# Kernel tuning notes

Hardware: AMD Instinct MI355X
Metric: run time of the kernel (lower is better)

The kernel has to match this reference:

```python
import jax, jax.numpy as jnp
import numpy as np

MODEL_DIM = 256
DK = 32        # dim_per_head
H = 16         # num_heads
HD = DK * H    # 512


def setup_inputs() -> dict:
    key = jax.random.key(0)
    ks = jax.random.split(key, 12)
    B, S = 16, 1024
    sc = 1.0 / np.sqrt(MODEL_DIM)
    inp = {
        "key0":   jax.random.normal(ks[0], (B, S, MODEL_DIM), jnp.float32),
        "value0": jax.random.normal(ks[1], (B, S, MODEL_DIM), jnp.float32),
        "query0": jax.random.normal(ks[2], (B, S, MODEL_DIM), jnp.float32),
        # linear weights stored as [in, out] (torch W.T)
        "Wk": jax.random.normal(ks[3], (MODEL_DIM, HD), jnp.float32) * sc,
        "bk": jax.random.normal(ks[4], (HD,), jnp.float32) * sc,
        "Wv": jax.random.normal(ks[5], (MODEL_DIM, HD), jnp.float32) * sc,
        "bv": jax.random.normal(ks[6], (HD,), jnp.float32) * sc,
        "Wq": jax.random.normal(ks[7], (MODEL_DIM, HD), jnp.float32) * sc,
        "bq": jax.random.normal(ks[8], (HD,), jnp.float32) * sc,
        "Wr": jax.random.normal(ks[9], (MODEL_DIM, HD), jnp.float32) * sc,
        "br": jax.random.normal(ks[10], (HD,), jnp.float32) * sc,
    }
    return inp


def reference(key0, value0, query0, Wk, bk, Wv, bv, Wq, bq, Wr, br):
    B = key0.shape[0]
    k = key0 @ Wk + bk      # [B, S, HD]
    v = value0 @ Wv + bv
    q = query0 @ Wq + bq
    # Faithful to the torch code: plain view (NO transpose) into (B*H, S, DK)
    k = k.reshape(B * H, -1, DK)
    v = v.reshape(B * H, -1, DK)
    q = q.reshape(B * H, -1, DK)
    # scale = (dk // num_heads) ** -0.5 = (32//16)**-0.5 (quirk preserved)
    scale = jnp.asarray((DK // H) ** (-0.5), k.dtype)
    attn = jax.nn.softmax(jnp.einsum("bqd,bkd->bqk", q, k) * scale, axis=2)
    context = jnp.einsum("bqk,bkd->bqd", attn, v)  # [B*H, S, DK]
    context = context.reshape(B, -1, HD)
    residual = (query0 @ Wr + br).reshape(B, -1, HD)
    return jax.nn.relu(residual + context)
```

## Files before the change

kernel.cpp:

```cpp
#include <hip/hip_runtime.h>
#include <hip/hip_bf16.h>

typedef _Float16 f16x8 __attribute__((ext_vector_type(8)));
typedef _Float16 f16x2 __attribute__((ext_vector_type(2)));
typedef float f32x4 __attribute__((ext_vector_type(4)));
typedef float f32x16 __attribute__((ext_vector_type(16)));
typedef unsigned int u32x2 __attribute__((ext_vector_type(2)));
typedef unsigned int u32x4 __attribute__((ext_vector_type(4)));
typedef unsigned short us8 __attribute__((ext_vector_type(8)));

#define GLDS16(gp, lp)                                                        \
  __builtin_amdgcn_global_load_lds(                                           \
      (const __attribute__((address_space(1))) void*)(gp),                    \
      (__attribute__((address_space(3))) void*)(lp), 16, 0, 0)

__device__ __forceinline__ unsigned short f2h(float f) {
  _Float16 h = (_Float16)f;
  return __builtin_bit_cast(unsigned short, h);
}
__device__ __forceinline__ float h2f(unsigned short u) {
  return (float)__builtin_bit_cast(_Float16, u);
}
__device__ __forceinline__ unsigned int pk2(float a, float b) {
  return __builtin_bit_cast(unsigned int, __builtin_amdgcn_cvt_pkrtz(a, b));
}

__global__ __launch_bounds__(256) void k_convert_w(
    const float* __restrict__ Wk, const float* __restrict__ Wv,
    const float* __restrict__ Wq, const float* __restrict__ Wr,
    unsigned short* __restrict__ WT) {
  int o = blockIdx.x * 256 + threadIdx.x;
  int mat = o >> 17, rem = o & 131071;
  int n = rem >> 8, k = rem & 255;
  const float* W = mat == 0 ? Wk : mat == 1 ? Wv : mat == 2 ? Wq : Wr;
  WT[o] = f2h(W[k * 512 + n]);
}

__global__ __launch_bounds__(1024) void k_gemm(
    const float* __restrict__ k0, const float* __restrict__ v0,
    const float* __restrict__ q0, const unsigned short* __restrict__ WT,
    const float* __restrict__ bk, const float* __restrict__ bv,
    const float* __restrict__ bq, const float* __restrict__ br,
    unsigned short* __restrict__ Kb, unsigned short* __restrict__ Vh,
    unsigned short* __restrict__ Qb, unsigned short* __restrict__ Rh) {
  const float CS = 0.70710678118654752f * 1.44269504088896341f;
  int b = blockIdx.x;
  int mat = b >> 7, my = b & 127;
  const float* A = mat == 0 ? k0 : mat == 1 ? v0 : q0;
  const unsigned short* Wm = WT + mat * 131072;
  const float* bias = mat == 0 ? bk : mat == 1 ? bv : mat == 2 ? bq : br;
  unsigned short* C = mat == 0 ? Kb : mat == 1 ? Vh : mat == 2 ? Qb : Rh;
  __shared__ __align__(16) unsigned short As[2][4096];
  __shared__ __align__(16) unsigned short Bs[2][16384];
  int m0 = my * 128;
  int tid = threadIdx.x, lane = tid & 63, w = tid >> 6;
  int wm = w >> 3, wn = w & 7, q = lane & 15, hi = lane >> 4;
  f32x4 acc[4][4];
#pragma unroll
  for (int i = 0; i < 4; ++i)
#pragma unroll
    for (int j = 0; j < 4; ++j) acc[i][j] = f32x4{0.f, 0.f, 0.f, 0.f};

  float bsv[4];
#pragma unroll
  for (int j = 0; j < 4; ++j) bsv[j] = bias[wn * 64 + j * 16 + q];

  const float* gA = A + (m0 + (tid >> 3)) * 256 + (tid & 7) * 4;
  const unsigned short* gB = Wm + (tid >> 2) * 256 + (tid & 3) * 8;

  float4 arF[2];
  arF[0] = *(const float4*)gA;
  arF[1] = *(const float4*)(gA + 32);
  GLDS16(gB, &Bs[0][tid * 8]);
  GLDS16(gB + 65536, &Bs[0][8192 + tid * 8]);
  asm volatile("s_waitcnt vmcnt(3)" ::: "memory");
  *(u32x2*)&As[0][tid * 4] =
      u32x2{pk2(arF[0].x, arF[0].y), pk2(arF[0].z, arF[0].w)};
  asm volatile("s_waitcnt lgkmcnt(0)" ::: "memory");
  __builtin_amdgcn_s_barrier();
  __builtin_amdgcn_sched_barrier(0);

#pragma unroll
  for (int kt = 0; kt < 8; ++kt) {
    int cur = kt & 1, nxt = cur ^ 1;
    if (kt < 6) arF[cur] = *(const float4*)(gA + (kt + 2) * 32);
    if (kt < 7) {
      GLDS16(gB + (kt + 1) * 32, &Bs[nxt][tid * 8]);
      GLDS16(gB + (kt + 1) * 32 + 65536, &Bs[nxt][8192 + tid * 8]);
    }
    if (kt < 6) asm volatile("s_waitcnt vmcnt(3)" ::: "memory");
    else if (kt == 6) asm volatile("s_waitcnt vmcnt(2)" ::: "memory");
    else asm volatile("s_waitcnt vmcnt(0)" ::: "memory");
    __builtin_amdgcn_s_barrier();
    __builtin_amdgcn_sched_barrier(0);

    f16x8 af[4], bf[4];
#pragma unroll
    for (int i = 0; i < 4; ++i)
      af[i] = *(const f16x8*)&As[cur][(wm * 64 + i * 16 + q) * 32 + hi * 8];
#pragma unroll
    for (int j = 0; j < 4; ++j)
      bf[j] = *(const f16x8*)&Bs[cur][(wn * 64 + j * 16 + q) * 32 + hi * 8];
#pragma unroll
    for (int i = 0; i < 4; ++i)
#pragma unroll
      for (int j = 0; j < 4; ++j)
        acc[i][j] = __builtin_amdgcn_mfma_f32_16x16x32_f16(af[i], bf[j], acc[i][j], 0, 0, 0);

    if (kt < 7) {
      *(u32x2*)&As[nxt][tid * 4] =
          u32x2{pk2(arF[nxt].x, arF[nxt].y), pk2(arF[nxt].z, arF[nxt].w)};
    }
    asm volatile("s_waitcnt lgkmcnt(0)" ::: "memory");
    __builtin_amdgcn_s_barrier();
    __builtin_amdgcn_sched_barrier(0);
  }

  float scale = (mat == 2) ? CS : 1.0f;
#pragma unroll
  for (int j = 0; j < 4; ++j) {
    int col = wn * 64 + j * 16 + q;
    float bs = bsv[j];
#pragma unroll
    for (int i = 0; i < 4; ++i) {
      int rb = m0 + wm * 64 + i * 16 + 4 * hi;
#pragma unroll
      for (int r = 0; r < 4; ++r) {
        float v = (acc[i][j][r] + bs) * scale;
        C[(rb + r) * 512 + col] = f2h(v);
      }
    }
  }
}

#define QK2(dst, kk0, kk1, qtl)                                               \
  dst = __builtin_amdgcn_mfma_f32_32x32x16_f16(kk0, qf[qtl][0], neg24, 0, 0, 0); \
  dst = __builtin_amdgcn_mfma_f32_32x32x16_f16(kk1, qf[qtl][1], dst, 0, 0, 0);

#define LOADKF(kv, blk, d0, d1)                                               \
  d0 = *(const f16x8*)(Ks + (kbase ^ 0) + (kv) * 4096 + (blk) * 2048);        \
  d1 = *(const f16x8*)(Ks + (kbase ^ 32) + (kv) * 4096 + (blk) * 2048);

#define LOADVF(kv, blk, d0, d1)                                               \
  d0 = *(const f16x8*)(Vs + ((vbase ^ ((2 * (blk)) << 5)) + (kv) * 128));     \
  d1 = *(const f16x8*)(Vs + ((vbase ^ ((2 * (blk) + 1) << 5)) + (kv) * 128));

#define PROC(st, qtl, vv0, vv1)                                               \
  {                                                                           \
    unsigned int w_[8];                                                       \
    _Pragma("unroll") for (int m = 0; m < 8; ++m) {                           \
      float p0_ = __builtin_amdgcn_exp2f(st[2 * m]);                          \
      float p1_ = __builtin_amdgcn_exp2f(st[2 * m + 1]);                      \
      w_[m] = pk2(p0_, p1_);                                                  \
    }                                                                         \
    _Pragma("unroll") for (int m = 0; m < 8; ++m)                             \
      lacc[qtl] = __builtin_amdgcn_fdot2(__builtin_bit_cast(f16x2, w_[m]),    \
                                         ones2, lacc[qtl], false);            \
    unsigned int a0_ = w_[0], a2_ = w_[2], a1_ = w_[1], a3_ = w_[3];          \
    unsigned int b0_ = w_[4], b2_ = w_[6], b1_ = w_[5], b3_ = w_[7];          \
    asm("v_permlane32_swap_b32 %0, %1" : "+v"(a0_), "+v"(a2_));               \
    asm("v_permlane32_swap_b32 %0, %1" : "+v"(a1_), "+v"(a3_));               \
    asm("v_permlane32_swap_b32 %0, %1" : "+v"(b0_), "+v"(b2_));               \
    asm("v_permlane32_swap_b32 %0, %1" : "+v"(b1_), "+v"(b3_));               \
    f16x8 pb0_ = __builtin_bit_cast(f16x8, (u32x4){a0_, a1_, a2_, a3_});      \
    f16x8 pb1_ = __builtin_bit_cast(f16x8, (u32x4){b0_, b1_, b2_, b3_});      \
    o[qtl] = __builtin_amdgcn_mfma_f32_32x32x16_f16(vv0, pb0_, o[qtl], 0, 0, 0); \
    o[qtl] = __builtin_amdgcn_mfma_f32_32x32x16_f16(vv1, pb1_, o[qtl], 0, 0, 0); \
  }

__global__ __launch_bounds__(1024) void k_attn(
    const unsigned short* __restrict__ Kb, const unsigned short* __restrict__ Vh,
    const unsigned short* __restrict__ Qb, const unsigned short* __restrict__ Rh,
    float* __restrict__ out) {
  __shared__ __align__(16) char Ks[65536];
  __shared__ __align__(16) char Vs[65536];

  int p = blockIdx.x;
  int g = (p & 7) * 32 + (p >> 3);
  int tid = threadIdx.x, lane = tid & 63, wid = tid >> 6;
  int q = lane & 31, h2 = lane >> 5;

  const char* Ksrc = (const char*)Kb + (size_t)g * 65536;
#pragma unroll
  for (int r = 0; r < 4; ++r) {
    int dk = tid * 16 + r * 16384;
    GLDS16(Ksrc + (dk ^ (((dk >> 7) & 7) << 4)), Ks + dk);
  }

  {
    const unsigned short* VhG = Vh + g * 32768;
    int d = tid & 31, s8b = tid >> 5;
#pragma unroll
    for (int it = 0; it < 4; ++it) {
      int s8 = s8b + it * 32;
      us8 v;
#pragma unroll
      for (int i = 0; i < 8; ++i) v[i] = VhG[(s8 * 8 + i) * 32 + d];
      *(us8*)(Vs + ((d * 2048 + s8 * 16) ^ ((d & 7) << 4))) = v;
    }
  }

  const unsigned short* Qg = Qb + g * 32768 + wid * 2048;
  f16x8 qf[2][2];
#pragma unroll
  for (int qt = 0; qt < 2; ++qt)
#pragma unroll
    for (int kh = 0; kh < 2; ++kh)
      qf[qt][kh] = *(const f16x8*)&Qg[(qt * 32 + q) * 32 + kh * 16 + h2 * 8];

  int kbase = (q * 64 + h2 * 16) ^ (((q >> 1) & 7) << 4);
  int vbase = (q * 2048 + h2 * 16) ^ ((q & 7) << 4);

  const f16x2 ones2 = {(_Float16)1.0f, (_Float16)1.0f};
  f32x16 o[2];
#pragma unroll
  for (int i = 0; i < 16; ++i) { o[0][i] = 0.f; o[1][i] = 0.f; }
  float lacc[2] = {0.f, 0.f};
  f32x16 neg24;
#pragma unroll
  for (int i = 0; i < 16; ++i) neg24[i] = -24.f;

  __syncthreads();

  f16x8 k0A, k1A, v0A, v1A, k0B, k1B, v0B, v1B;
  f32x16 stA, s1, s2, s3;
  LOADKF(0, 0, k0A, k1A);
  LOADVF(0, 0, v0A, v1A);
  QK2(stA, k0A, k1A, 0);

  for (int kv = 0; kv < 16; ++kv) {
    QK2(s1, k0A, k1A, 1);
    PROC(stA, 0, v0A, v1A);
    LOADKF(kv, 1, k0B, k1B);
    LOADVF(kv, 1, v0B, v1B);
    QK2(s2, k0B, k1B, 0);
    PROC(s1, 1, v0A, v1A);
    QK2(s3, k0B, k1B, 1);
    PROC(s2, 0, v0B, v1B);
    if (kv < 15) {
      LOADKF(kv + 1, 0, k0A, k1A);
      LOADVF(kv + 1, 0, v0A, v1A);
      QK2(stA, k0A, k1A, 0);
    }
    PROC(s3, 1, v0B, v1B);
  }

#pragma unroll
  for (int qt = 0; qt < 2; ++qt)
    lacc[qt] += __shfl_xor(lacc[qt], 32, 64);

#pragma unroll
  for (int qt = 0; qt < 2; ++qt) {
    float iv = 1.0f / lacc[qt];
    int rowoff = g * 32768 + (wid * 64 + qt * 32 + q) * 32;
#pragma unroll
    for (int rg = 0; rg < 4; ++rg) {
      int off = rowoff + rg * 8 + h2 * 4;
      ushort4 rr = *(const ushort4*)&Rh[off];
      float4 ov;
      ov.x = fmaxf(h2f(rr.x) + o[qt][4 * rg + 0] * iv, 0.f);
      ov.y = fmaxf(h2f(rr.y) + o[qt][4 * rg + 1] * iv, 0.f);
      ov.z = fmaxf(h2f(rr.z) + o[qt][4 * rg + 2] * iv, 0.f);
      ov.w = fmaxf(h2f(rr.w) + o[qt][4 * rg + 3] * iv, 0.f);
      *(float4*)&out[off] = ov;
    }
  }
}

extern "C" void kernel_launch(void* const* d_in, const int* in_sizes, int n_in,
                              void* d_out, int out_size, void* d_ws, size_t ws_size,
                              hipStream_t stream) {
  const float* key0 = (const float*)d_in[0];
  const float* value0 = (const float*)d_in[1];
  const float* query0 = (const float*)d_in[2];
  const float* Wk = (const float*)d_in[3];
  const float* bk = (const float*)d_in[4];
  const float* Wv = (const float*)d_in[5];
  const float* bv = (const float*)d_in[6];
  const float* Wq = (const float*)d_in[7];
  const float* bq = (const float*)d_in[8];
  const float* Wr = (const float*)d_in[9];
  const float* br = (const float*)d_in[10];
  float* out = (float*)d_out;
  char* ws = (char*)d_ws;
  unsigned short* Kb = (unsigned short*)(ws);
  unsigned short* Vh = (unsigned short*)(ws + 16777216);
  unsigned short* Qb = (unsigned short*)(ws + 33554432);
  unsigned short* Rh = (unsigned short*)(ws + 50331648);
  unsigned short* WT = (unsigned short*)(ws + 92274688);

  k_convert_w<<<dim3(2048), dim3(256), 0, stream>>>(Wk, Wv, Wq, Wr, WT);
  k_gemm<<<dim3(512), dim3(1024), 0, stream>>>(key0, value0, query0, WT,
                                               bk, bv, bq, br, Kb, Vh, Qb, Rh);
  k_attn<<<dim3(256), dim3(1024), 0, stream>>>(Kb, Vh, Qb, Rh, out);
}
```

Measured before the change: 96.57 us.

## Split projection GEMM into 512-thread half-N tiles with deeper B prefetch

The projection GEMM now uses 1024 blocks of 512 threads, each covering 128 rows by 256 output columns instead of all 512. The B tile is held in a 4-stage ring buffer and prefetched two k-steps ahead. The per-step barrier before the MFMAs is removed, and block IDs are remapped so adjacent blocks spread across matrices. The aim is better occupancy and latency hiding for the global loads, at the cost of loading each A tile twice (once per column half).

```diff
diff --git a/kernel.cpp b/kernel.cpp
--- a/kernel.cpp
+++ b/kernel.cpp
@@ -13,6 +13,8 @@
   __builtin_amdgcn_global_load_lds(                                           \
       (const __attribute__((address_space(1))) void*)(gp),                    \
       (__attribute__((address_space(3))) void*)(lp), 16, 0, 0)
+
+#define MEMFENCE asm volatile("" ::: "memory")
 
 __device__ __forceinline__ unsigned short f2h(float f) {
   _Float16 h = (_Float16)f;
@@ -36,7 +38,7 @@
   WT[o] = f2h(W[k * 512 + n]);
 }
 
-__global__ __launch_bounds__(1024) void k_gemm(
+__global__ __launch_bounds__(512) void k_gemm(
     const float* __restrict__ k0, const float* __restrict__ v0,
     const float* __restrict__ q0, const unsigned short* __restrict__ WT,
     const float* __restrict__ bk, const float* __restrict__ bv,
@@ -45,16 +47,17 @@
     unsigned short* __restrict__ Qb, unsigned short* __restrict__ Rh) {
   const float CS = 0.70710678118654752f * 1.44269504088896341f;
   int b = blockIdx.x;
-  int mat = b >> 7, my = b & 127;
+  int id2 = (b & 7) * 128 + (b >> 3);
+  int mat = id2 >> 8, rest = id2 & 255, my = rest >> 1, nx = rest & 1;
   const float* A = mat == 0 ? k0 : mat == 1 ? v0 : q0;
   const unsigned short* Wm = WT + mat * 131072;
   const float* bias = mat == 0 ? bk : mat == 1 ? bv : mat == 2 ? bq : br;
   unsigned short* C = mat == 0 ? Kb : mat == 1 ? Vh : mat == 2 ? Qb : Rh;
   __shared__ __align__(16) unsigned short As[2][4096];
-  __shared__ __align__(16) unsigned short Bs[2][16384];
-  int m0 = my * 128;
+  __shared__ __align__(16) unsigned short Bs[4][8192];
+  int m0 = my * 128, n0 = nx * 256;
   int tid = threadIdx.x, lane = tid & 63, w = tid >> 6;
-  int wm = w >> 3, wn = w & 7, q = lane & 15, hi = lane >> 4;
+  int wm = w >> 2, wn = w & 3, q = lane & 15, hi = lane >> 4;
   f32x4 acc[4][4];
 #pragma unroll
   for (int i = 0; i < 4; ++i)
@@ -63,19 +66,34 @@
 
   float bsv[4];
 #pragma unroll
-  for (int j = 0; j < 4; ++j) bsv[j] = bias[wn * 64 + j * 16 + q];
-
-  const float* gA = A + (m0 + (tid >> 3)) * 256 + (tid & 7) * 4;
-  const unsigned short* gB = Wm + (tid >> 2) * 256 + (tid & 3) * 8;
-
-  float4 arF[2];
-  arF[0] = *(const float4*)gA;
-  arF[1] = *(const float4*)(gA + 32);
-  GLDS16(gB, &Bs[0][tid * 8]);
-  GLDS16(gB + 65536, &Bs[0][8192 + tid * 8]);
-  asm volatile("s_waitcnt vmcnt(3)" ::: "memory");
-  *(u32x2*)&As[0][tid * 4] =
-      u32x2{pk2(arF[0].x, arF[0].y), pk2(arF[0].z, arF[0].w)};
+  for (int j = 0; j < 4; ++j) bsv[j] = bias[n0 + wn * 64 + j * 16 + q];
+  MEMFENCE;
+
+  int c0 = tid, c1 = 512 + tid;
+  const unsigned short* gB0 = Wm + (n0 + (c0 >> 2)) * 256 + (c0 & 3) * 8;
+  const unsigned short* gB1 = Wm + (n0 + (c1 >> 2)) * 256 + (c1 & 3) * 8;
+  char* BsB = (char*)&Bs[0][0];
+  const float* gA = A + (m0 + (tid >> 2)) * 256 + (tid & 3) * 8;
+  int aoff = (tid >> 2) * 64 + (tid & 3) * 16;
+  float4 aA[2], aB[2];
+
+  GLDS16(gB0, BsB + c0 * 16);
+  GLDS16(gB1, BsB + c1 * 16);
+  MEMFENCE;
+  aA[0] = *(const float4*)gA;
+  aB[0] = *(const float4*)(gA + 4);
+  MEMFENCE;
+  GLDS16(gB0 + 32, BsB + 16384 + c0 * 16);
+  GLDS16(gB1 + 32, BsB + 16384 + c1 * 16);
+  MEMFENCE;
+  aA[1] = *(const float4*)(gA + 32);
+  aB[1] = *(const float4*)(gA + 36);
+  asm volatile("s_waitcnt vmcnt(4)" ::: "memory");
+  {
+    u32x4 wv = {pk2(aA[0].x, aA[0].y), pk2(aA[0].z, aA[0].w),
+                pk2(aB[0].x, aB[0].y), pk2(aB[0].z, aB[0].w)};
+    *(u32x4*)((char*)&As[0][0] + aoff) = wv;
+  }
   asm volatile("s_waitcnt lgkmcnt(0)" ::: "memory");
   __builtin_amdgcn_s_barrier();
   __builtin_amdgcn_sched_barrier(0);
@@ -83,24 +101,24 @@
 #pragma unroll
   for (int kt = 0; kt < 8; ++kt) {
     int cur = kt & 1, nxt = cur ^ 1;
-    if (kt < 6) arF[cur] = *(const float4*)(gA + (kt + 2) * 32);
-    if (kt < 7) {
-      GLDS16(gB + (kt + 1) * 32, &Bs[nxt][tid * 8]);
-      GLDS16(gB + (kt + 1) * 32 + 65536, &Bs[nxt][8192 + tid * 8]);
-    }
-    if (kt < 6) asm volatile("s_waitcnt vmcnt(3)" ::: "memory");
-    else if (kt == 6) asm volatile("s_waitcnt vmcnt(2)" ::: "memory");
-    else asm volatile("s_waitcnt vmcnt(0)" ::: "memory");
-    __builtin_amdgcn_s_barrier();
-    __builtin_amdgcn_sched_barrier(0);
+    if (kt <= 5) {
+      GLDS16(gB0 + (kt + 2) * 32, BsB + ((kt + 2) & 3) * 16384 + c0 * 16);
+      GLDS16(gB1 + (kt + 2) * 32, BsB + ((kt + 2) & 3) * 16384 + c1 * 16);
+      MEMFENCE;
+      aA[cur] = *(const float4*)(gA + (kt + 2) * 32);
+      aB[cur] = *(const float4*)(gA + (kt + 2) * 32 + 4);
+      MEMFENCE;
+    }
 
     f16x8 af[4], bf[4];
 #pragma unroll
     for (int i = 0; i < 4; ++i)
-      af[i] = *(const f16x8*)&As[cur][(wm * 64 + i * 16 + q) * 32 + hi * 8];
+      af[i] = *(const f16x8*)((char*)&As[cur][0] +
+                              (wm * 64 + i * 16 + q) * 64 + hi * 16);
 #pragma unroll
     for (int j = 0; j < 4; ++j)
-      bf[j] = *(const f16x8*)&Bs[cur][(wn * 64 + j * 16 + q) * 32 + hi * 8];
+      bf[j] = *(const f16x8*)(BsB + (kt & 3) * 16384 +
+                              (wn * 64 + j * 16 + q) * 64 + hi * 16);
 #pragma unroll
     for (int i = 0; i < 4; ++i)
 #pragma unroll
@@ -108,8 +126,11 @@
         acc[i][j] = __builtin_amdgcn_mfma_f32_16x16x32_f16(af[i], bf[j], acc[i][j], 0, 0, 0);
 
     if (kt < 7) {
-      *(u32x2*)&As[nxt][tid * 4] =
-          u32x2{pk2(arF[nxt].x, arF[nxt].y), pk2(arF[nxt].z, arF[nxt].w)};
+      if (kt <= 5) asm volatile("s_waitcnt vmcnt(4)" ::: "memory");
+      else asm volatile("s_waitcnt vmcnt(0)" ::: "memory");
+      u32x4 wv = {pk2(aA[nxt].x, aA[nxt].y), pk2(aA[nxt].z, aA[nxt].w),
+                  pk2(aB[nxt].x, aB[nxt].y), pk2(aB[nxt].z, aB[nxt].w)};
+      *(u32x4*)((char*)&As[nxt][0] + aoff) = wv;
     }
     asm volatile("s_waitcnt lgkmcnt(0)" ::: "memory");
     __builtin_amdgcn_s_barrier();
@@ -119,7 +140,7 @@
   float scale = (mat == 2) ? CS : 1.0f;
 #pragma unroll
   for (int j = 0; j < 4; ++j) {
-    int col = wn * 64 + j * 16 + q;
+    int col = n0 + wn * 64 + j * 16 + q;
     float bs = bsv[j];
 #pragma unroll
     for (int i = 0; i < 4; ++i) {
@@ -290,7 +311,7 @@
   unsigned short* WT = (unsigned short*)(ws + 92274688);
 
   k_convert_w<<<dim3(2048), dim3(256), 0, stream>>>(Wk, Wv, Wq, Wr, WT);
-  k_gemm<<<dim3(512), dim3(1024), 0, stream>>>(key0, value0, query0, WT,
+  k_gemm<<<dim3(1024), dim3(512), 0, stream>>>(key0, value0, query0, WT,
                                                bk, bv, bq, br, Kb, Vh, Qb, Rh);
   k_attn<<<dim3(256), dim3(1024), 0, stream>>>(Kb, Vh, Qb, Rh, out);
 }
```

New measurement: 99.64 us. 3.2% more time.
